# Kernel optimization log

Hardware: AMD Instinct MI355X
Metric: run time of the kernel (lower is better)

Reference implementation:

```python
import jax, jax.numpy as jnp
import numpy as np

N = 100000          # total nodes
G = 128             # number of graphs
D_IN, D_H, D_OUT = 512, 1024, 512
E = 1600000         # edges (unused by the math, matches forward signature)


def setup_inputs() -> dict:
    key = jax.random.key(0)
    ks = jax.random.split(key, 9)
    x = jax.random.normal(ks[0], (N, D_IN), dtype=jnp.float32)
    edge_index = jax.random.randint(ks[1], (2, E), 0, N, dtype=jnp.int64)
    # sorted batch ids; guarantee every graph id appears at least once
    batch = jnp.sort(jnp.concatenate([
        jnp.arange(G, dtype=jnp.int64),
        jax.random.randint(ks[2], (N - G,), 0, G, dtype=jnp.int64),
    ]))
    s = 0.02
    W0 = jax.random.normal(ks[3], (D_IN, D_H), dtype=jnp.float32) * s
    b0 = jnp.zeros((D_H,), dtype=jnp.float32)
    W1 = jax.random.normal(ks[4], (D_H, D_H), dtype=jnp.float32) * s
    b1 = jnp.zeros((D_H,), dtype=jnp.float32)
    W2 = jax.random.normal(ks[5], (D_H, D_OUT), dtype=jnp.float32) * s
    b2 = jnp.zeros((D_OUT,), dtype=jnp.float32)
    return {"x": x, "edge_index": edge_index, "batch": batch,
            "W0": W0, "b0": b0, "W1": W1, "b1": b1, "W2": W2, "b2": b2}


def reference(x, edge_index, batch, W0, b0, W1, b1, W2, b2):
    # Linear + ReLU stack (dropout p=0 -> identity in eval). edge_index is unused,
    # matching the original module (its 'GCN' layer is a plain nn.Linear).
    h = jax.nn.relu(x @ W0 + b0)
    h = jax.nn.relu(h @ W1 + b1)
    h = jax.nn.relu(h @ W2 + b2)        # [N, D_OUT]
    # global mean pool per graph: fused segment-sum replaces the per-graph mask loop
    sums = jax.ops.segment_sum(h, batch, num_segments=G)                 # [G, D_OUT]
    counts = jax.ops.segment_sum(jnp.ones((h.shape[0],), h.dtype), batch,
                                 num_segments=G)                          # [G]
    return sums / counts[:, None]
```

## Files before the change

### kernel.cpp

```cpp
#include <hip/hip_runtime.h>
#include <cstdint>
#include <cstddef>

typedef __bf16 bf16x8 __attribute__((ext_vector_type(8)));
typedef float f32x4 __attribute__((ext_vector_type(4)));

__device__ __forceinline__ unsigned short f2bf(float f) {
  unsigned u = __float_as_uint(f);
  u += 0x7fffu + ((u >> 16) & 1u);
  return (unsigned short)(u >> 16);
}
__device__ __forceinline__ float bf2f(unsigned short s) {
  return __uint_as_float(((unsigned)s) << 16);
}

__device__ __forceinline__ void gld_lds16(const void* g, void* l) {
  __builtin_amdgcn_global_load_lds(
      (const __attribute__((address_space(1))) void*)g,
      (__attribute__((address_space(3))) void*)l, 16, 0, 0);
}

#define BARM() do { __builtin_amdgcn_s_barrier(); asm volatile("" ::: "memory"); } while (0)
#define VMCNT(n) asm volatile("s_waitcnt vmcnt(" #n ")" ::: "memory")
#define LGKMW() asm volatile("s_waitcnt lgkmcnt(0)" ::: "memory")

__global__ void transpose_w(const float* __restrict__ w, unsigned short* __restrict__ wt,
                            int K, int N) {
  __shared__ float tile[32][33];
  int nt = N >> 5;
  int bx = blockIdx.x % nt;
  int by = blockIdx.x / nt;
  int tx = threadIdx.x & 31, ty = threadIdx.x >> 5;
#pragma unroll
  for (int r = 0; r < 32; r += 8)
    tile[ty + r][tx] = w[(size_t)(by * 32 + ty + r) * N + bx * 32 + tx];
  __syncthreads();
#pragma unroll
  for (int r = 0; r < 32; r += 8)
    wt[(size_t)(bx * 32 + ty + r) * K + by * 32 + tx] = f2bf(tile[tx][ty + r]);
}

__global__ void cvt_x(const float* __restrict__ x, unsigned short* __restrict__ xb,
                      int rows, int nvalid, int D) {
  size_t total = (size_t)rows * D / 8;
  for (size_t i = (size_t)blockIdx.x * blockDim.x + threadIdx.x; i < total;
       i += (size_t)gridDim.x * blockDim.x) {
    size_t e = i * 8;
    int row = (int)(e / (size_t)D);
    uint4 ov;
    if (row < nvalid) {
      const float4* s = (const float4*)(x + e);
      float4 v0 = s[0], v1 = s[1];
      ov.x = (unsigned)f2bf(v0.x) | ((unsigned)f2bf(v0.y) << 16);
      ov.y = (unsigned)f2bf(v0.z) | ((unsigned)f2bf(v0.w) << 16);
      ov.z = (unsigned)f2bf(v1.x) | ((unsigned)f2bf(v1.y) << 16);
      ov.w = (unsigned)f2bf(v1.z) | ((unsigned)f2bf(v1.w) << 16);
    } else {
      ov.x = ov.y = ov.z = ov.w = 0u;
    }
    *(uint4*)(xb + e) = ov;
  }
}

__device__ __forceinline__ bf16x8 read_frag(const unsigned short* region, int row, int kel) {
  int ke = kel ^ (((row >> 1) & 3) << 3);
  return *(const bf16x8*)(region + row * 32 + ke);
}

__device__ __forceinline__ void stage_half(const unsigned short* gpanel, int K, int kofs,
                                           unsigned short* region, int tid) {
  int row = tid >> 2;
  int ke = ((tid & 3) * 8) ^ (((row >> 1) & 3) << 3);
  gld_lds16(gpanel + (size_t)row * K + kofs + ke, region + tid * 8);
}

#define MFMA16X(BV)                                                             \
  _Pragma("unroll") for (int mm = 0; mm < 4; ++mm)                              \
      _Pragma("unroll") for (int nn = 0; nn < 4; ++nn)                          \
          acc[mm][nn] = __builtin_amdgcn_mfma_f32_16x16x32_bf16(                \
              av[mm], BV[nn], acc[mm][nn], 0, 0, 0)

#define GEMM_PREAMBLE_AND_KLOOP()                                               \
  const int tid = threadIdx.x;                                                  \
  const int w = tid >> 6, l = tid & 63;                                         \
  const int wm = w >> 2, wn = w & 3;                                            \
  const int lc = l & 15, lk8 = (l >> 4) * 8;                                    \
  const int nbn = N >> 8;                                                       \
  const int nwg = gridDim.x;                                                    \
  const int q = nwg >> 3, rr = nwg & 7;                                         \
  const int xcd = blockIdx.x & 7, ib = blockIdx.x >> 3;                         \
  const int bswz = (xcd < rr ? xcd * (q + 1) : rr * (q + 1) + (xcd - rr) * q) + ib; \
  const int bm = bswz / nbn, bn = bswz - bm * nbn;                              \
  const unsigned short* Ap = A + (size_t)bm * 256 * K;                          \
  const unsigned short* Bp = Bt + (size_t)bn * 256 * K;                         \
  const int T = K >> 6;                                                         \
  f32x4 acc[4][4] = {};                                                         \
  stage_half(Ap, K, 0, &lds[0][0][0][0][0], tid);                               \
  stage_half(Bp, K, 0, &lds[0][1][0][0][0], tid);                               \
  stage_half(Ap, K, 32, &lds[0][0][1][0][0], tid);                              \
  stage_half(Bp, K, 32, &lds[0][1][1][0][0], tid);                              \
  VMCNT(0);                                                                     \
  BARM();                                                                       \
  for (int t = 0; t < T; ++t) {                                                 \
    const int s = t & 1;                                                        \
    const unsigned short* Ak0 = &lds[s][0][0][0][0];                            \
    const unsigned short* Ak1 = &lds[s][0][1][0][0];                            \
    const unsigned short* Bk0 = &lds[s][1][0][0][0];                            \
    const unsigned short* Bk1 = &lds[s][1][1][0][0];                            \
    unsigned short* nAk0 = &lds[s ^ 1][0][0][0][0];                             \
    unsigned short* nBk0 = &lds[s ^ 1][1][0][0][0];                             \
    unsigned short* nAk1 = &lds[s ^ 1][0][1][0][0];                             \
    unsigned short* nBk1 = &lds[s ^ 1][1][1][0][0];                             \
    bf16x8 av[4], bq[4];                                                        \
    if (t + 1 < T) {                                                            \
      stage_half(Ap, K, (t + 1) * 64, nAk0, tid);                               \
      stage_half(Bp, K, (t + 1) * 64, nBk0, tid);                               \
      stage_half(Ap, K, (t + 1) * 64 + 32, nAk1, tid);                          \
      stage_half(Bp, K, (t + 1) * 64 + 32, nBk1, tid);                          \
    }                                                                           \
                                                     \
    _Pragma("unroll") for (int mm = 0; mm < 4; ++mm)                            \
        av[mm] = read_frag(Ak0, wm * 64 + mm * 16 + lc, lk8);                   \
    _Pragma("unroll") for (int nn = 0; nn < 4; ++nn)                            \
        bq[nn] = read_frag(Bk0, wn * 64 + nn * 16 + lc, lk8);                   \
    MFMA16X(bq);                                                                \
                                                     \
    _Pragma("unroll") for (int mm = 0; mm < 4; ++mm)                            \
        av[mm] = read_frag(Ak1, wm * 64 + mm * 16 + lc, lk8);                   \
    _Pragma("unroll") for (int nn = 0; nn < 4; ++nn)                            \
        bq[nn] = read_frag(Bk1, wn * 64 + nn * 16 + lc, lk8);                   \
    MFMA16X(bq);                                                                \
    LGKMW();                             \
    VMCNT(0);              \
    BARM();                             \
  }

__global__ __launch_bounds__(1024, 1) void gemm256(
    const unsigned short* __restrict__ A,
    const unsigned short* __restrict__ Bt,
    const float* __restrict__ bias,
    unsigned short* __restrict__ C,
    int N, int K) {
  __shared__ alignas(16) unsigned short lds[2][2][2][256][32];
  GEMM_PREAMBLE_AND_KLOOP();

  unsigned short* eps = &lds[0][0][0][0][0];
  float bv[4];
#pragma unroll
  for (int nn = 0; nn < 4; ++nn) bv[nn] = bias[bn * 256 + wn * 64 + nn * 16 + lc];

#pragma unroll
  for (int r = 0; r < 2; ++r) {
    if ((wm >> 1) == r) {
#pragma unroll
      for (int mm = 0; mm < 4; ++mm) {
#pragma unroll
        for (int nn = 0; nn < 4; ++nn) {
          int lcol = wn * 64 + nn * 16 + lc;
#pragma unroll
          for (int j = 0; j < 4; ++j) {
            int lrow = (wm & 1) * 64 + mm * 16 + (l >> 4) * 4 + j;
            float v = fmaxf(acc[mm][nn][j] + bv[nn], 0.0f);
            eps[lrow * 256 + (lcol ^ (((lrow >> 2) & 3) << 4))] = f2bf(v);
          }
        }
      }
    }
    BARM();
#pragma unroll
    for (int it = 0; it < 4; ++it) {
      int flat = it * 1024 + tid;
      int lrow = flat >> 5, cb = flat & 31;
      int ce = (cb * 8) ^ (((lrow >> 2) & 3) << 4);
      uint4 v = *(const uint4*)&eps[lrow * 256 + ce];
      *(uint4*)&C[(size_t)(bm * 256 + r * 128 + lrow) * N + bn * 256 + cb * 8] = v;
    }
    BARM();
  }
}

__global__ __launch_bounds__(1024, 1) void gemm_pool(
    const unsigned short* __restrict__ A,
    const unsigned short* __restrict__ Bt,
    const float* __restrict__ bias,
    const int* __restrict__ batch,
    float* __restrict__ part,
    int N, int K, int row0, int Nn) {
  __shared__ alignas(16) unsigned short lds[2][2][2][256][32];
  GEMM_PREAMBLE_AND_KLOOP();

  unsigned short* eps = &lds[0][0][0][0][0];
  int* batchLS = (int*)&lds[1][0][0][0][0];
  if (tid < 256) {
    int grow = row0 + bm * 256 + tid;
    batchLS[tid] = (grow < Nn) ? batch[grow] : -1;
  }
  float bv[4];
#pragma unroll
  for (int nn = 0; nn < 4; ++nn) bv[nn] = bias[bn * 256 + wn * 64 + nn * 16 + lc];

#pragma unroll
  for (int r = 0; r < 2; ++r) {
    if ((wm >> 1) == r) {
#pragma unroll
      for (int mm = 0; mm < 4; ++mm) {
#pragma unroll
        for (int nn = 0; nn < 4; ++nn) {
          int lcol = wn * 64 + nn * 16 + lc;
#pragma unroll
          for (int j = 0; j < 4; ++j) {
            int lrow = (wm & 1) * 64 + mm * 16 + (l >> 4) * 4 + j;
            float v = fmaxf(acc[mm][nn][j] + bv[nn], 0.0f);
            eps[lrow * 256 + (lcol ^ (((lrow >> 2) & 3) << 4))] = f2bf(v);
          }
        }
      }
    }
    BARM();
    {
      int col = tid & 255;
      int qt = tid >> 8;
      int gcur = -2;
      float run = 0.f;
      int gcolbase = bn * 256 + col;
      for (int i = 0; i < 32; ++i) {
        int lr = qt * 32 + i;
        int g = batchLS[r * 128 + lr];
        if (g != gcur) {
          if (gcur >= 0) atomicAdd(&part[(size_t)gcur * N + gcolbase], run);
          gcur = g; run = 0.f;
        }
        run += bf2f(eps[lr * 256 + (col ^ (((lr >> 2) & 3) << 4))]);
      }
      if (gcur >= 0) atomicAdd(&part[(size_t)gcur * N + gcolbase], run);
    }
    BARM();
  }
}

__global__ void zero_part(float* __restrict__ part, int n) {
  int i = blockIdx.x * blockDim.x + threadIdx.x;
  if (i < n) part[i] = 0.f;
}

__global__ void pool_div(const float* __restrict__ part, const int* __restrict__ batch,
                         float* __restrict__ out, int n, int D, int G) {
  int idx = blockIdx.x * blockDim.x + threadIdx.x;
  if (idx >= G * D) return;
  int g = idx / D;
  int lo, hi;
  { int a = 0, b = n; while (a < b) { int m = (a + b) >> 1; if (batch[m] < g) a = m + 1; else b = m; } lo = a; }
  { int a = lo, b = n; while (a < b) { int m = (a + b) >> 1; if (batch[m] < g + 1) a = m + 1; else b = m; } hi = a; }
  out[idx] = part[idx] / (float)(hi - lo);
}

static inline size_t align256(size_t x) { return (x + 255) & ~(size_t)255; }

extern "C" void kernel_launch(void* const* d_in, const int* in_sizes, int n_in,
                              void* d_out, int out_size, void* d_ws, size_t ws_size,
                              hipStream_t stream) {
  const float* x = (const float*)d_in[0];
  const int* batch = (const int*)d_in[2];
  const float* W0 = (const float*)d_in[3];
  const float* b0 = (const float*)d_in[4];
  const float* W1 = (const float*)d_in[5];
  const float* b1 = (const float*)d_in[6];
  const float* W2 = (const float*)d_in[7];
  const float* b2 = (const float*)d_in[8];
  float* out = (float*)d_out;

  const int Nn = in_sizes[2];
  const int DIN = 512, DH = 1024, DOUT = 512;
  const int G = out_size / DOUT;
  const int Mpad = ((Nn + 255) / 256) * 256;

  uint8_t* p = (uint8_t*)d_ws;
  unsigned short* W0t = (unsigned short*)p; p += align256((size_t)DH * DIN * 2);
  unsigned short* W1t = (unsigned short*)p; p += align256((size_t)DH * DH * 2);
  unsigned short* W2t = (unsigned short*)p; p += align256((size_t)DOUT * DH * 2);
  float* part         = (float*)p;          p += align256((size_t)G * DOUT * 4);
  size_t used = (size_t)(p - (uint8_t*)d_ws);
  size_t avail = ws_size > used ? ws_size - used : 0;
  size_t per_row = (size_t)(DIN + DH + DH) * 2;
  long long chl = (long long)(avail / per_row);
  chl = (chl / 256) * 256;
  int CH = (int)(chl < 256 ? 256 : chl);
  if (CH > Mpad) CH = Mpad;
  unsigned short* xb = (unsigned short*)p; p += align256((size_t)CH * DIN * 2);
  unsigned short* h0 = (unsigned short*)p; p += align256((size_t)CH * DH * 2);
  unsigned short* h1 = (unsigned short*)p; p += align256((size_t)CH * DH * 2);

  zero_part<<<dim3((G * DOUT + 255) / 256), 256, 0, stream>>>(part, G * DOUT);

  transpose_w<<<dim3((DIN / 32) * (DH / 32)), 256, 0, stream>>>(W0, W0t, DIN, DH);
  transpose_w<<<dim3((DH / 32) * (DH / 32)), 256, 0, stream>>>(W1, W1t, DH, DH);
  transpose_w<<<dim3((DH / 32) * (DOUT / 32)), 256, 0, stream>>>(W2, W2t, DH, DOUT);

  for (int off = 0; off < Mpad; off += CH) {
    int rows = Mpad - off; if (rows > CH) rows = CH;
    int nvalid = Nn - off;
    size_t cvt_threads = (size_t)rows * DIN / 8;
    int cvt_blocks = (int)((cvt_threads + 255) / 256);
    if (cvt_blocks > 2048) cvt_blocks = 2048;
    cvt_x<<<dim3(cvt_blocks), 256, 0, stream>>>(x + (size_t)off * DIN, xb, rows, nvalid, DIN);

    gemm256<<<dim3((rows / 256) * (DH / 256)), 1024, 0, stream>>>(xb, W0t, b0, h0, DH, DIN);
    gemm256<<<dim3((rows / 256) * (DH / 256)), 1024, 0, stream>>>(h0, W1t, b1, h1, DH, DH);
    gemm_pool<<<dim3((rows / 256) * (DOUT / 256)), 1024, 0, stream>>>(
        h1, W2t, b2, batch, part, DOUT, DH, off, Nn);
  }

  pool_div<<<dim3((G * DOUT + 255) / 256), 256, 0, stream>>>(part, batch, out, Nn, DOUT, G);
}
```

Measured before the change: 660.6 us.

## Switch GEMMs to 256x128 tiles with 512 threads and triple-buffered K pipeline

```diff
diff --git a/kernel.cpp b/kernel.cpp
--- a/kernel.cpp
+++ b/kernel.cpp
@@ -67,11 +67,20 @@
   return *(const bf16x8*)(region + row * 32 + ke);
 }
 
-__device__ __forceinline__ void stage_half(const unsigned short* gpanel, int K, int kofs,
-                                           unsigned short* region, int tid) {
+__device__ __forceinline__ void stage_a(const unsigned short* gp, int K, int kofs,
+                                        unsigned short* region, int tid) {
+#pragma unroll
+  for (int r = 0; r < 2; ++r) {
+    int row = r * 128 + (tid >> 2);
+    int ke = ((tid & 3) * 8) ^ (((row >> 1) & 3) << 3);
+    gld_lds16(gp + (size_t)row * K + kofs + ke, region + r * 4096 + tid * 8);
+  }
+}
+__device__ __forceinline__ void stage_b(const unsigned short* gp, int K, int kofs,
+                                        unsigned short* region, int tid) {
   int row = tid >> 2;
   int ke = ((tid & 3) * 8) ^ (((row >> 1) & 3) << 3);
-  gld_lds16(gpanel + (size_t)row * K + kofs + ke, region + tid * 8);
+  gld_lds16(gp + (size_t)row * K + kofs + ke, region + tid * 8);
 }
 
 #define MFMA16X(BV)                                                             \
@@ -83,71 +92,60 @@
 #define GEMM_PREAMBLE_AND_KLOOP()                                               \
   const int tid = threadIdx.x;                                                  \
   const int w = tid >> 6, l = tid & 63;                                         \
-  const int wm = w >> 2, wn = w & 3;                                            \
+  const int wm = w >> 1, wn = w & 1;                                            \
   const int lc = l & 15, lk8 = (l >> 4) * 8;                                    \
-  const int nbn = N >> 8;                                                       \
+  const int nbn = N >> 7;                                                       \
   const int nwg = gridDim.x;                                                    \
   const int q = nwg >> 3, rr = nwg & 7;                                         \
   const int xcd = blockIdx.x & 7, ib = blockIdx.x >> 3;                         \
   const int bswz = (xcd < rr ? xcd * (q + 1) : rr * (q + 1) + (xcd - rr) * q) + ib; \
   const int bm = bswz / nbn, bn = bswz - bm * nbn;                              \
   const unsigned short* Ap = A + (size_t)bm * 256 * K;                          \
-  const unsigned short* Bp = Bt + (size_t)bn * 256 * K;                         \
-  const int T = K >> 6;                                                         \
+  const unsigned short* Bp = Bt + (size_t)bn * 128 * K;                         \
+  const int T = K >> 5;                                                         \
   f32x4 acc[4][4] = {};                                                         \
-  stage_half(Ap, K, 0, &lds[0][0][0][0][0], tid);                               \
-  stage_half(Bp, K, 0, &lds[0][1][0][0][0], tid);                               \
-  stage_half(Ap, K, 32, &lds[0][0][1][0][0], tid);                              \
-  stage_half(Bp, K, 32, &lds[0][1][1][0][0], tid);                              \
-  VMCNT(0);                                                                     \
+  stage_a(Ap, K, 0, &lds[0][0], tid);                                           \
+  stage_b(Bp, K, 0, &lds[0][8192], tid);                                        \
+  stage_a(Ap, K, 32, &lds[1][0], tid);                                          \
+  stage_b(Bp, K, 32, &lds[1][8192], tid);                                       \
+  VMCNT(3);                     \
   BARM();                                                                       \
-  for (int t = 0; t < T; ++t) {                                                 \
-    const int s = t & 1;                                                        \
-    const unsigned short* Ak0 = &lds[s][0][0][0][0];                            \
-    const unsigned short* Ak1 = &lds[s][0][1][0][0];                            \
-    const unsigned short* Bk0 = &lds[s][1][0][0][0];                            \
-    const unsigned short* Bk1 = &lds[s][1][1][0][0];                            \
-    unsigned short* nAk0 = &lds[s ^ 1][0][0][0][0];                             \
-    unsigned short* nBk0 = &lds[s ^ 1][1][0][0][0];                             \
-    unsigned short* nAk1 = &lds[s ^ 1][0][1][0][0];                             \
-    unsigned short* nBk1 = &lds[s ^ 1][1][1][0][0];                             \
-    bf16x8 av[4], bq[4];                                                        \
-    if (t + 1 < T) {                                                            \
-      stage_half(Ap, K, (t + 1) * 64, nAk0, tid);                               \
-      stage_half(Bp, K, (t + 1) * 64, nBk0, tid);                               \
-      stage_half(Ap, K, (t + 1) * 64 + 32, nAk1, tid);                          \
-      stage_half(Bp, K, (t + 1) * 64 + 32, nBk1, tid);                          \
+  {                                                                             \
+    int s = 0, sp = 2;         \
+    for (int t = 0; t < T; ++t) {                                               \
+      const unsigned short* As = &lds[s][0];                                    \
+      const unsigned short* Bs = &lds[s][8192];                                 \
+      bf16x8 av[4], bq[4];                                                      \
+      _Pragma("unroll") for (int mm = 0; mm < 4; ++mm)                          \
+          av[mm] = read_frag(As, wm * 64 + mm * 16 + lc, lk8);                  \
+      _Pragma("unroll") for (int nn = 0; nn < 4; ++nn)                          \
+          bq[nn] = read_frag(Bs, wn * 64 + nn * 16 + lc, lk8);                  \
+      if (t + 2 < T) {                                                          \
+        stage_a(Ap, K, (t + 2) * 32, &lds[sp][0], tid);                         \
+        stage_b(Bp, K, (t + 2) * 32, &lds[sp][8192], tid);                      \
+      }                                                                         \
+      MFMA16X(bq);                                                              \
+      LGKMW();                           \
+      if (t + 2 < T) { VMCNT(3); } else { VMCNT(0); }                           \
+      BARM();                              \
+      sp = s;                                                                   \
+      s = (s == 2) ? 0 : s + 1;                                                 \
     }                                                                           \
-                                                     \
-    _Pragma("unroll") for (int mm = 0; mm < 4; ++mm)                            \
-        av[mm] = read_frag(Ak0, wm * 64 + mm * 16 + lc, lk8);                   \
-    _Pragma("unroll") for (int nn = 0; nn < 4; ++nn)                            \
-        bq[nn] = read_frag(Bk0, wn * 64 + nn * 16 + lc, lk8);                   \
-    MFMA16X(bq);                                                                \
-                                                     \
-    _Pragma("unroll") for (int mm = 0; mm < 4; ++mm)                            \
-        av[mm] = read_frag(Ak1, wm * 64 + mm * 16 + lc, lk8);                   \
-    _Pragma("unroll") for (int nn = 0; nn < 4; ++nn)                            \
-        bq[nn] = read_frag(Bk1, wn * 64 + nn * 16 + lc, lk8);                   \
-    MFMA16X(bq);                                                                \
-    LGKMW();                             \
-    VMCNT(0);              \
-    BARM();                             \
-  }
-
-__global__ __launch_bounds__(1024, 1) void gemm256(
+  }
+
+__global__ __launch_bounds__(512, 4) void gemm256(
     const unsigned short* __restrict__ A,
     const unsigned short* __restrict__ Bt,
     const float* __restrict__ bias,
     unsigned short* __restrict__ C,
     int N, int K) {
-  __shared__ alignas(16) unsigned short lds[2][2][2][256][32];
+  __shared__ alignas(16) unsigned short lds[3][12288];
   GEMM_PREAMBLE_AND_KLOOP();
 
-  unsigned short* eps = &lds[0][0][0][0][0];
+  unsigned short* eps = &lds[0][0];
   float bv[4];
 #pragma unroll
-  for (int nn = 0; nn < 4; ++nn) bv[nn] = bias[bn * 256 + wn * 64 + nn * 16 + lc];
+  for (int nn = 0; nn < 4; ++nn) bv[nn] = bias[bn * 128 + wn * 64 + nn * 16 + lc];
 
 #pragma unroll
   for (int r = 0; r < 2; ++r) {
@@ -161,7 +159,7 @@
           for (int j = 0; j < 4; ++j) {
             int lrow = (wm & 1) * 64 + mm * 16 + (l >> 4) * 4 + j;
             float v = fmaxf(acc[mm][nn][j] + bv[nn], 0.0f);
-            eps[lrow * 256 + (lcol ^ (((lrow >> 2) & 3) << 4))] = f2bf(v);
+            eps[lrow * 136 + lcol] = f2bf(v);
           }
         }
       }
@@ -169,35 +167,34 @@
     BARM();
 #pragma unroll
     for (int it = 0; it < 4; ++it) {
-      int flat = it * 1024 + tid;
-      int lrow = flat >> 5, cb = flat & 31;
-      int ce = (cb * 8) ^ (((lrow >> 2) & 3) << 4);
-      uint4 v = *(const uint4*)&eps[lrow * 256 + ce];
-      *(uint4*)&C[(size_t)(bm * 256 + r * 128 + lrow) * N + bn * 256 + cb * 8] = v;
+      int flat = it * 512 + tid;
+      int lrow = flat >> 4, cb = flat & 15;
+      uint4 v = *(const uint4*)&eps[lrow * 136 + cb * 8];
+      *(uint4*)&C[(size_t)(bm * 256 + r * 128 + lrow) * N + bn * 128 + cb * 8] = v;
     }
     BARM();
   }
 }
 
-__global__ __launch_bounds__(1024, 1) void gemm_pool(
+__global__ __launch_bounds__(512, 4) void gemm_pool(
     const unsigned short* __restrict__ A,
     const unsigned short* __restrict__ Bt,
     const float* __restrict__ bias,
     const int* __restrict__ batch,
     float* __restrict__ part,
     int N, int K, int row0, int Nn) {
-  __shared__ alignas(16) unsigned short lds[2][2][2][256][32];
+  __shared__ alignas(16) unsigned short lds[3][12288];
+  __shared__ int batchLS[256];
   GEMM_PREAMBLE_AND_KLOOP();
 
-  unsigned short* eps = &lds[0][0][0][0][0];
-  int* batchLS = (int*)&lds[1][0][0][0][0];
+  unsigned short* eps = &lds[0][0];
   if (tid < 256) {
     int grow = row0 + bm * 256 + tid;
     batchLS[tid] = (grow < Nn) ? batch[grow] : -1;
   }
   float bv[4];
 #pragma unroll
-  for (int nn = 0; nn < 4; ++nn) bv[nn] = bias[bn * 256 + wn * 64 + nn * 16 + lc];
+  for (int nn = 0; nn < 4; ++nn) bv[nn] = bias[bn * 128 + wn * 64 + nn * 16 + lc];
 
 #pragma unroll
   for (int r = 0; r < 2; ++r) {
@@ -211,18 +208,18 @@
           for (int j = 0; j < 4; ++j) {
             int lrow = (wm & 1) * 64 + mm * 16 + (l >> 4) * 4 + j;
             float v = fmaxf(acc[mm][nn][j] + bv[nn], 0.0f);
-            eps[lrow * 256 + (lcol ^ (((lrow >> 2) & 3) << 4))] = f2bf(v);
+            eps[lrow * 136 + lcol] = f2bf(v);
           }
         }
       }
     }
     BARM();
     {
-      int col = tid & 255;
-      int qt = tid >> 8;
+      int col = tid & 127;
+      int qt = tid >> 7;
       int gcur = -2;
       float run = 0.f;
-      int gcolbase = bn * 256 + col;
+      int gcolbase = bn * 128 + col;
       for (int i = 0; i < 32; ++i) {
         int lr = qt * 32 + i;
         int g = batchLS[r * 128 + lr];
@@ -230,7 +227,7 @@
           if (gcur >= 0) atomicAdd(&part[(size_t)gcur * N + gcolbase], run);
           gcur = g; run = 0.f;
         }
-        run += bf2f(eps[lr * 256 + (col ^ (((lr >> 2) & 3) << 4))]);
+        run += bf2f(eps[lr * 136 + col]);
       }
       if (gcur >= 0) atomicAdd(&part[(size_t)gcur * N + gcolbase], run);
     }
@@ -304,9 +301,9 @@
     if (cvt_blocks > 2048) cvt_blocks = 2048;
     cvt_x<<<dim3(cvt_blocks), 256, 0, stream>>>(x + (size_t)off * DIN, xb, rows, nvalid, DIN);
 
-    gemm256<<<dim3((rows / 256) * (DH / 256)), 1024, 0, stream>>>(xb, W0t, b0, h0, DH, DIN);
-    gemm256<<<dim3((rows / 256) * (DH / 256)), 1024, 0, stream>>>(h0, W1t, b1, h1, DH, DH);
-    gemm_pool<<<dim3((rows / 256) * (DOUT / 256)), 1024, 0, stream>>>(
+    gemm256<<<dim3((rows / 256) * (DH / 128)), 512, 0, stream>>>(xb, W0t, b0, h0, DH, DIN);
+    gemm256<<<dim3((rows / 256) * (DH / 128)), 512, 0, stream>>>(h0, W1t, b1, h1, DH, DH);
+    gemm_pool<<<dim3((rows / 256) * (DOUT / 128)), 512, 0, stream>>>(
         h1, W2t, b2, batch, part, DOUT, DH, off, Nn);
   }
 
```

After: 614.4 us. 7.0% less time.
